# Optimization experiments

Measured on AMD Instinct MI355X. Metric: run time of the kernel, lower is better.

## Reference

```python
import jax, jax.numpy as jnp
from jax import lax
import numpy as np


def fourier_kernel(coef, xs):
    """Evaluate the real Fourier kernel. coef: (n, idim, odim); xs: (...,).
    Returns (..., idim, odim). Matches torch version: complex exp split into cos/sin,
    interior modes doubled."""
    n = coef.shape[0]
    mh = n // 2 + 1
    rr = coef[:mh]                                   # cosine coeffs (mh, i, o)
    ii = jnp.zeros_like(rr).at[1:n - mh + 1].set(jnp.flip(coef[mh:], axis=0))
    k = 2.0 * jnp.pi * jnp.arange(mh, dtype=xs.dtype)
    ang = k * xs[..., None]                          # (..., mh)
    scale = jnp.ones((mh,), dtype=xs.dtype).at[1:-1].set(2.0)
    cr = jnp.cos(ang) * scale
    si = jnp.sin(ang) * scale
    return jnp.tensordot(cr, rr, 1) - jnp.tensordot(si, ii, 1)


def sem_conv(nodal, coef, ws, grid, ndim, dim):
    """Windowed spectral-element convolution along direction `dim`.
    nodal: (m_0..m_{ndim-1}, E_0..E_{ndim-1}, idim); ws: (s+1, m, m); grid: (m,)."""
    ns = ''.join(chr(120 + i) for i in range(ndim))          # node axes: 'xy'
    o = ns[dim].upper()
    ms = ns.replace(ns[dim], o)
    es = ''.join(chr(97 + i) for i in range(ndim))           # element axes: 'ab'
    eqn = f'{ns}{es}i,{o}{ns[dim]}io,{o}{ns[dim]}->{ms}{es}o'
    ax = ndim + dim                                          # element axis for `dim`
    E = nodal.shape[ax]
    s1 = ws.shape[0]
    r = s1 // 2
    # circular padding along element axis (matches [pad_l, nodal, pad_r])
    pad_l = lax.slice_in_dim(nodal, E - r, E, axis=ax)
    pad_r = lax.slice_in_dim(nodal, 0, r, axis=ax)
    f = jnp.concatenate([pad_l, nodal, pad_r], axis=ax)
    out = None
    for k in range(s1):                                      # small fixed window loop
        xy = (grid[:, None] - (grid[None, :] + (k - r))) / (s1 - 1)   # (m, m)
        g = fourier_kernel(coef, xy)                         # (m, m, idim, odim)
        fx = lax.slice_in_dim(f, k, k + E, axis=ax)
        term = jnp.einsum(eqn, fx, g, ws[k])
        out = term if out is None else out + term
    return out


def setup_inputs() -> dict:
    key = jax.random.key(0)
    k1, k2, k3, k4, k5 = jax.random.split(key, 5)
    m, E, idim, odim, mode, s = 8, 144, 16, 16, 16, 4
    nodal = jax.random.normal(k1, (m, m, E, E, idim), dtype=jnp.float32)
    coef0 = jax.random.normal(k2, (s * mode, idim, odim), dtype=jnp.float32) * 0.02
    coef1 = jax.random.normal(k3, (s * mode, idim, odim), dtype=jnp.float32) * 0.02
    ws0 = jax.random.normal(k4, (s + 1, m, m), dtype=jnp.float32) * 0.1
    ws1 = jax.random.normal(k5, (s + 1, m, m), dtype=jnp.float32) * 0.1
    grid = jnp.linspace(0.0, 1.0, m, dtype=jnp.float32)
    return {"nodal": nodal, "coef0": coef0, "coef1": coef1,
            "ws0": ws0, "ws1": ws1, "grid": grid}


def reference(nodal, coef0, coef1, ws0, ws1, grid):
    # SEMConv.__call__: sum of factorized convolutions over each spatial dim
    return (sem_conv(nodal, coef0, ws0, grid, 2, 0)
            + sem_conv(nodal, coef1, ws1, grid, 2, 1))
```

## Files before the change

kernel.cpp:

```cpp
#include <hip/hip_runtime.h>

typedef __attribute__((ext_vector_type(8))) short short8;
typedef __attribute__((ext_vector_type(4))) float f32x4;

#define NODAL_ELEMS 21233664
#define BSLAB 81920
#define NB_OFF 327680

__device__ __forceinline__ unsigned short f2bf(float f) {
    unsigned int u = __float_as_uint(f);
    u += 0x7FFFu + ((u >> 16) & 1u);
    return (unsigned short)(u >> 16);
}

__device__ __forceinline__ void gload_lds16(const void* g, void* l) {
    __builtin_amdgcn_global_load_lds(
        (const __attribute__((address_space(1))) unsigned int*)g,
        (__attribute__((address_space(3))) unsigned int*)l, 16, 0, 0);
}

__global__ void build_b_kernel(const float* __restrict__ coef0,
                               const float* __restrict__ coef1,
                               const float* __restrict__ ws0,
                               const float* __restrict__ ws1,
                               const float* __restrict__ grid,
                               unsigned short* __restrict__ B)
{
    const int bid = blockIdx.x;
    const int d   = (bid >= 320) ? 1 : 0;
    const int rem = bid - d * 320;
    const int k   = rem >> 6;
    const int X   = (rem >> 3) & 7;
    const int x   = rem & 7;

    const float* __restrict__ coef = d ? coef1 : coef0;
    const float* __restrict__ ws   = d ? ws1 : ws0;
    unsigned short* __restrict__ Bd = B + d * BSLAB;

    const float xy = (grid[X] - (grid[x] + (float)(k - 2))) * 0.25f;
    const int t = threadIdx.x;
    const int i = t >> 4;
    const int o = t & 15;

    float acc = 0.f;
    #pragma unroll 1
    for (int j = 0; j < 33; ++j) {
        float ang = 6.283185307179586f * (float)j * xy;
        float c = cosf(ang);
        float s = sinf(ang);
        float sc = (j == 0 || j == 32) ? 1.f : 2.f;
        float rr = coef[j * 256 + t];
        float ii = (j >= 1 && j <= 31) ? coef[(64 - j) * 256 + t] : 0.f;
        acc += sc * (c * rr - s * ii);
    }
    float val = acc * ws[(k * 8 + X) * 8 + x];

    const int kk = k * 16 + x * 2 + (i >> 3);
    const int jj = i & 7;
    const int n  = X * 16 + o;
    Bd[(kk * 128 + n) * 8 + jj] = f2bf(val);
}

__global__ void cvt_kernel(const float* __restrict__ in,
                           unsigned short* __restrict__ out, int n4)
{
    int idx = blockIdx.x * blockDim.x + threadIdx.x;
    int stride = gridDim.x * blockDim.x;
    for (int j = idx; j < n4; j += stride) {
        float4 v = ((const float4*)in)[j];
        ushort4 r;
        r.x = f2bf(v.x); r.y = f2bf(v.y); r.z = f2bf(v.z); r.w = f2bf(v.w);
        ((ushort4*)out)[j] = r;
    }
}

template<int TERM, bool AB16>
__global__ __launch_bounds__(256, 3)
void conv_mfma(const float* __restrict__ nodalf,
               const unsigned short* __restrict__ nodalb,
               const unsigned short* __restrict__ Bmat,
               float* __restrict__ out)
{
    __shared__ __align__(16) char lds[2][16384];

    const int tid = threadIdx.x;
    const int w   = tid >> 6;
    const int l   = tid & 63;
    const int sub = l >> 4;
    const int lr  = l & 15;

    const int bid  = blockIdx.x;
    const int XF   = bid & 7;
    const int rest = bid >> 3;
    const int half = (rest >= 81) ? 1 : 0;
    const int mt   = rest - half * 81;

    const int scal = (TERM == 0) ? XF * 331776 : XF * 2654208;
    const int KSTR = (TERM == 0) ? 2654208 : 331776;

    int base[2][5];
    const int rowbase = mt * 128 + w * 32;
    #pragma unroll
    for (int mf = 0; mf < 2; ++mf) {
        int row = rowbase + mf * 16 + lr;
        int a = row / 72;
        int b = row - a * 72 + half * 72;
        #pragma unroll
        for (int k = 0; k < 5; ++k) {
            int sh = ((TERM == 0) ? a : b) + k - 2;
            if (sh < 0) sh += 144;
            if (sh >= 144) sh -= 144;
            int off = (TERM == 0) ? (sh * 2304 + b * 16) : (a * 2304 + sh * 16);
            base[mf][k] = off + (sub >> 1) * KSTR + (sub & 1) * 8;
        }
    }

    const unsigned short* nb = nodalb + scal;
    const float* nfp = nodalf + scal;
    const char* Bb = (const char*)Bmat;

    f32x4 acc[2][8];
    #pragma unroll
    for (int mf = 0; mf < 2; ++mf)
        #pragma unroll
        for (int nf = 0; nf < 8; ++nf)
            acc[mf][nf] = (f32x4){0.f, 0.f, 0.f, 0.f};

    short8 Ab[2][2][2];
    float4 Af[2][2][2][2];

#define STAGE_B(buf_, c_) do {                                               \
    _Pragma("unroll")                                                        \
    for (int u_ = 0; u_ < 4; ++u_)                                           \
        gload_lds16(Bb + (c_) * 16384 + u_ * 4096 + tid * 16,                \
                    &lds[buf_][u_ * 4096 + tid * 16]);                       \
} while (0)

#define LOAD_A(slot_, c_) do {                                               \
    _Pragma("unroll")                                                        \
    for (int ksp_ = 0; ksp_ < 2; ++ksp_) {                                   \
        const int ks_ = 2 * (c_) + ksp_;                                     \
        _Pragma("unroll")                                                    \
        for (int mf_ = 0; mf_ < 2; ++mf_) {                                  \
            if (AB16) {                                                      \
                Ab[slot_][ksp_][mf_] = *(const short8*)                      \
                    (nb + base[mf_][ks_ >> 2] + (ks_ & 3) * 2 * KSTR);       \
            } else {                                                         \
                const float* s_ = nfp + base[mf_][ks_ >> 2]                  \
                                      + (ks_ & 3) * 2 * KSTR;                \
                Af[slot_][ksp_][mf_][0] = *(const float4*)s_;                \
                Af[slot_][ksp_][mf_][1] = *(const float4*)(s_ + 4);          \
            }                                                                \
        }                                                                    \
    } } while (0)

#define CHUNK_BARRIER() do {                                                 \
    __builtin_amdgcn_sched_barrier(0);                                       \
    asm volatile("s_waitcnt vmcnt(4)" ::: "memory");                         \
    __builtin_amdgcn_s_barrier();                                            \
    __builtin_amdgcn_sched_barrier(0);                                       \
} while (0)

    STAGE_B(0, 0);
    __builtin_amdgcn_sched_barrier(0);
    LOAD_A(0, 0);
    CHUNK_BARRIER();

    #pragma unroll
    for (int c = 0; c < 10; ++c) {
        if (c < 9) {
            STAGE_B((c + 1) & 1, c + 1);
            __builtin_amdgcn_sched_barrier(0);
            LOAD_A((c + 1) & 1, c + 1);
            __builtin_amdgcn_sched_barrier(0);
        }

        #pragma unroll
        for (int ksp = 0; ksp < 2; ++ksp) {
            short8 a0, a1;
            if (AB16) {
                a0 = Ab[c & 1][ksp][0];
                a1 = Ab[c & 1][ksp][1];
            } else {
                #pragma unroll
                for (int e = 0; e < 4; ++e) {
                    a0[e]     = (short)f2bf(((const float*)&Af[c & 1][ksp][0][0])[e]);
                    a0[e + 4] = (short)f2bf(((const float*)&Af[c & 1][ksp][0][1])[e]);
                    a1[e]     = (short)f2bf(((const float*)&Af[c & 1][ksp][1][0])[e]);
                    a1[e + 4] = (short)f2bf(((const float*)&Af[c & 1][ksp][1][1])[e]);
                }
            }

            const char* bbase = lds[c & 1] + ksp * 8192 + sub * 2048 + lr * 16;
            #pragma unroll
            for (int nf = 0; nf < 8; ++nf) {
                short8 bf = *(const short8*)(bbase + nf * 256);
                acc[0][nf] = __builtin_amdgcn_mfma_f32_16x16x32_bf16(
                    a0, bf, acc[0][nf], 0, 0, 0);
                acc[1][nf] = __builtin_amdgcn_mfma_f32_16x16x32_bf16(
                    a1, bf, acc[1][nf], 0, 0, 0);
            }
        }

        if (c < 9) CHUNK_BARRIER();
    }

    #pragma unroll
    for (int mf = 0; mf < 2; ++mf) {
        #pragma unroll
        for (int r = 0; r < 4; ++r) {
            int row = rowbase + mf * 16 + sub * 4 + r;
            int a = row / 72;
            int b = row - a * 72 + half * 72;
            int ab16i = (a * 144 + b) * 16;
            #pragma unroll
            for (int nf = 0; nf < 8; ++nf) {
                int pq = (TERM == 0) ? (nf * 2654208 + XF * 331776)
                                     : (XF * 2654208 + nf * 331776);
                float v = acc[mf][nf][r];
                float* dst = out + pq + ab16i + lr;
                if (TERM == 0) *dst = v;
                else           *dst += v;
            }
        }
    }
#undef STAGE_B
#undef LOAD_A
#undef CHUNK_BARRIER
}

extern "C" void kernel_launch(void* const* d_in, const int* in_sizes, int n_in,
                              void* d_out, int out_size, void* d_ws, size_t ws_size,
                              hipStream_t stream) {
    const float* nodal = (const float*)d_in[0];
    const float* coef0 = (const float*)d_in[1];
    const float* coef1 = (const float*)d_in[2];
    const float* ws0   = (const float*)d_in[3];
    const float* ws1   = (const float*)d_in[4];
    const float* grid  = (const float*)d_in[5];
    float* outp = (float*)d_out;

    unsigned short* B      = (unsigned short*)d_ws;
    unsigned short* nodalb = (unsigned short*)((char*)d_ws + NB_OFF);
    const bool ab16 = ws_size >= (size_t)NB_OFF + (size_t)NODAL_ELEMS * 2;

    hipLaunchKernelGGL(build_b_kernel, dim3(640), dim3(256), 0, stream,
                       coef0, coef1, ws0, ws1, grid, B);
    if (ab16)
        hipLaunchKernelGGL(cvt_kernel, dim3(2048), dim3(256), 0, stream,
                           nodal, nodalb, NODAL_ELEMS / 4);

    dim3 g(1296);
    if (ab16) {
        hipLaunchKernelGGL((conv_mfma<0, true>), g, dim3(256), 0, stream,
                           nodal, nodalb, B, outp);
        hipLaunchKernelGGL((conv_mfma<1, true>), g, dim3(256), 0, stream,
                           nodal, nodalb, B + BSLAB, outp);
    } else {
        hipLaunchKernelGGL((conv_mfma<0, false>), g, dim3(256), 0, stream,
                           nodal, nodalb, B, outp);
        hipLaunchKernelGGL((conv_mfma<1, false>), g, dim3(256), 0, stream,
                           nodal, nodalb, B + BSLAB, outp);
    }
}
```

Before: 127.7 us.

## Triple-buffer B/A staging, raise MFMA priority, store term-0 partial in bf16

Deepens the software pipeline from double to triple buffering for both the LDS B tiles and the register A fragments, prefetching two chunks ahead and adjusting the vmcnt waits. MFMA blocks are wrapped in s_setprio to favor matrix issue. The first term's partial output is written as bf16 to workspace and read back by the second term, halving that intermediate traffic. The costs are more LDS and registers, which can lower occupancy, and extra rounding error on the intermediate sum.

```diff
diff --git a/kernel.cpp b/kernel.cpp
--- a/kernel.cpp
+++ b/kernel.cpp
@@ -6,11 +6,15 @@
 #define NODAL_ELEMS 21233664
 #define BSLAB 81920
 #define NB_OFF 327680
+#define C0_OFF (NB_OFF + (size_t)NODAL_ELEMS * 2)
 
 __device__ __forceinline__ unsigned short f2bf(float f) {
     unsigned int u = __float_as_uint(f);
     u += 0x7FFFu + ((u >> 16) & 1u);
     return (unsigned short)(u >> 16);
+}
+__device__ __forceinline__ float bf2f(unsigned short s) {
+    return __uint_as_float(((unsigned int)s) << 16);
 }
 
 __device__ __forceinline__ void gload_lds16(const void* g, void* l) {
@@ -74,14 +78,15 @@
     }
 }
 
-template<int TERM, bool AB16>
+template<int TERM, bool AB16, bool C0B16>
 __global__ __launch_bounds__(256, 3)
 void conv_mfma(const float* __restrict__ nodalf,
                const unsigned short* __restrict__ nodalb,
                const unsigned short* __restrict__ Bmat,
+               unsigned short* __restrict__ c0,
                float* __restrict__ out)
 {
-    __shared__ __align__(16) char lds[2][16384];
+    __shared__ __align__(16) char lds[3][16384];
 
     const int tid = threadIdx.x;
     const int w   = tid >> 6;
@@ -126,8 +131,8 @@
         for (int nf = 0; nf < 8; ++nf)
             acc[mf][nf] = (f32x4){0.f, 0.f, 0.f, 0.f};
 
-    short8 Ab[2][2][2];
-    float4 Af[2][2][2][2];
+    short8 Ab[3][2][2];
+    float4 Af[3][2][2][2];
 
 #define STAGE_B(buf_, c_) do {                                               \
     _Pragma("unroll")                                                        \
@@ -154,24 +159,26 @@
         }                                                                    \
     } } while (0)
 
-#define CHUNK_BARRIER() do {                                                 \
+#define CHUNK_BARRIER(vm_) do {                                              \
     __builtin_amdgcn_sched_barrier(0);                                       \
-    asm volatile("s_waitcnt vmcnt(4)" ::: "memory");                         \
+    asm volatile("s_waitcnt vmcnt(" vm_ ")" ::: "memory");                   \
     __builtin_amdgcn_s_barrier();                                            \
     __builtin_amdgcn_sched_barrier(0);                                       \
 } while (0)
 
     STAGE_B(0, 0);
+    STAGE_B(1, 1);
     __builtin_amdgcn_sched_barrier(0);
     LOAD_A(0, 0);
-    CHUNK_BARRIER();
+    LOAD_A(1, 1);
+    CHUNK_BARRIER("8");
 
     #pragma unroll
     for (int c = 0; c < 10; ++c) {
-        if (c < 9) {
-            STAGE_B((c + 1) & 1, c + 1);
+        if (c < 8) {
+            STAGE_B((c + 2) % 3, c + 2);
             __builtin_amdgcn_sched_barrier(0);
-            LOAD_A((c + 1) & 1, c + 1);
+            LOAD_A((c + 2) % 3, c + 2);
             __builtin_amdgcn_sched_barrier(0);
         }
 
@@ -179,19 +186,20 @@
         for (int ksp = 0; ksp < 2; ++ksp) {
             short8 a0, a1;
             if (AB16) {
-                a0 = Ab[c & 1][ksp][0];
-                a1 = Ab[c & 1][ksp][1];
+                a0 = Ab[c % 3][ksp][0];
+                a1 = Ab[c % 3][ksp][1];
             } else {
                 #pragma unroll
                 for (int e = 0; e < 4; ++e) {
-                    a0[e]     = (short)f2bf(((const float*)&Af[c & 1][ksp][0][0])[e]);
-                    a0[e + 4] = (short)f2bf(((const float*)&Af[c & 1][ksp][0][1])[e]);
-                    a1[e]     = (short)f2bf(((const float*)&Af[c & 1][ksp][1][0])[e]);
-                    a1[e + 4] = (short)f2bf(((const float*)&Af[c & 1][ksp][1][1])[e]);
+                    a0[e]     = (short)f2bf(((const float*)&Af[c % 3][ksp][0][0])[e]);
+                    a0[e + 4] = (short)f2bf(((const float*)&Af[c % 3][ksp][0][1])[e]);
+                    a1[e]     = (short)f2bf(((const float*)&Af[c % 3][ksp][1][0])[e]);
+                    a1[e + 4] = (short)f2bf(((const float*)&Af[c % 3][ksp][1][1])[e]);
                 }
             }
 
-            const char* bbase = lds[c & 1] + ksp * 8192 + sub * 2048 + lr * 16;
+            const char* bbase = lds[c % 3] + ksp * 8192 + sub * 2048 + lr * 16;
+            __builtin_amdgcn_s_setprio(1);
             #pragma unroll
             for (int nf = 0; nf < 8; ++nf) {
                 short8 bf = *(const short8*)(bbase + nf * 256);
@@ -200,9 +208,13 @@
                 acc[1][nf] = __builtin_amdgcn_mfma_f32_16x16x32_bf16(
                     a1, bf, acc[1][nf], 0, 0, 0);
             }
-        }
-
-        if (c < 9) CHUNK_BARRIER();
+            __builtin_amdgcn_s_setprio(0);
+        }
+
+        if (c < 9) {
+            if (c >= 8) CHUNK_BARRIER("0");
+            else        CHUNK_BARRIER("8");
+        }
     }
 
     #pragma unroll
@@ -217,10 +229,15 @@
             for (int nf = 0; nf < 8; ++nf) {
                 int pq = (TERM == 0) ? (nf * 2654208 + XF * 331776)
                                      : (XF * 2654208 + nf * 331776);
+                int idx = pq + ab16i + lr;
                 float v = acc[mf][nf][r];
-                float* dst = out + pq + ab16i + lr;
-                if (TERM == 0) *dst = v;
-                else           *dst += v;
+                if (TERM == 0) {
+                    if (C0B16) c0[idx] = f2bf(v);
+                    else       out[idx] = v;
+                } else {
+                    if (C0B16) out[idx] = v + bf2f(c0[idx]);
+                    else       out[idx] += v;
+                }
             }
         }
     }
@@ -242,7 +259,9 @@
 
     unsigned short* B      = (unsigned short*)d_ws;
     unsigned short* nodalb = (unsigned short*)((char*)d_ws + NB_OFF);
+    unsigned short* c0     = (unsigned short*)((char*)d_ws + C0_OFF);
     const bool ab16 = ws_size >= (size_t)NB_OFF + (size_t)NODAL_ELEMS * 2;
+    const bool c0b  = ws_size >= C0_OFF + (size_t)NODAL_ELEMS * 2;
 
     hipLaunchKernelGGL(build_b_kernel, dim3(640), dim3(256), 0, stream,
                        coef0, coef1, ws0, ws1, grid, B);
@@ -251,15 +270,20 @@
                            nodal, nodalb, NODAL_ELEMS / 4);
 
     dim3 g(1296);
-    if (ab16) {
-        hipLaunchKernelGGL((conv_mfma<0, true>), g, dim3(256), 0, stream,
-                           nodal, nodalb, B, outp);
-        hipLaunchKernelGGL((conv_mfma<1, true>), g, dim3(256), 0, stream,
-                           nodal, nodalb, B + BSLAB, outp);
+    if (ab16 && c0b) {
+        hipLaunchKernelGGL((conv_mfma<0, true, true>), g, dim3(256), 0, stream,
+                           nodal, nodalb, B, c0, outp);
+        hipLaunchKernelGGL((conv_mfma<1, true, true>), g, dim3(256), 0, stream,
+                           nodal, nodalb, B + BSLAB, c0, outp);
+    } else if (ab16) {
+        hipLaunchKernelGGL((conv_mfma<0, true, false>), g, dim3(256), 0, stream,
+                           nodal, nodalb, B, c0, outp);
+        hipLaunchKernelGGL((conv_mfma<1, true, false>), g, dim3(256), 0, stream,
+                           nodal, nodalb, B + BSLAB, c0, outp);
     } else {
-        hipLaunchKernelGGL((conv_mfma<0, false>), g, dim3(256), 0, stream,
-                           nodal, nodalb, B, outp);
-        hipLaunchKernelGGL((conv_mfma<1, false>), g, dim3(256), 0, stream,
-                           nodal, nodalb, B + BSLAB, outp);
-    }
-}
+        hipLaunchKernelGGL((conv_mfma<0, false, false>), g, dim3(256), 0, stream,
+                           nodal, nodalb, B, c0, outp);
+        hipLaunchKernelGGL((conv_mfma<1, false, false>), g, dim3(256), 0, stream,
+                           nodal, nodalb, B + BSLAB, c0, outp);
+    }
+}
```

Measured after the change: 119.6 us. -6.3%, faster.
